# Optimization experiments

Measured on AMD Instinct MI355X. Metric: run time of the kernel, lower is better.

The kernel has to match this reference:

```python
import jax, jax.numpy as jnp
import numpy as np
from jax import lax

EMBED = 200
HID = 300
NCLASS = 2
B = 64
S = 255          # complete binary tree: 2**8 - 1 nodes
DEPTH = 8        # levels 0..7, root at node 0
VOCAB = 32000


def make_tree():
    parent = np.zeros(S, np.int32)
    parent[0] = S  # sentinel: root has no parent (dropped via dummy segment)
    for i in range(1, S):
        parent[i] = (i - 1) // 2
    depth = np.floor(np.log2(np.arange(S) + 1)).astype(np.int32)
    return jnp.asarray(parent), jnp.asarray(depth)


def setup_inputs() -> dict:
    key = jax.random.key(0)
    ks = jax.random.split(key, 8)
    parent, depth = make_tree()
    return {
        "x": jax.random.randint(ks[0], (S, B), 0, VOCAB, dtype=jnp.int32),
        "parent": parent,
        "depth": depth,
        "embed": jax.random.normal(ks[1], (VOCAB, EMBED), jnp.float32) * 0.1,
        "W_iou": jax.random.normal(ks[2], (EMBED, 3 * HID), jnp.float32) * 0.05,
        "U_iou": jax.random.normal(ks[3], (HID, 3 * HID), jnp.float32) * 0.05,
        "b_iou": jnp.zeros((3 * HID,), jnp.float32),
        "W_f": jax.random.normal(ks[4], (EMBED, HID), jnp.float32) * 0.05,
        "U_f": jax.random.normal(ks[5], (HID, HID), jnp.float32) * 0.05,
        "b_f": jnp.zeros((HID,), jnp.float32),
        "W_out": jax.random.normal(ks[6], (HID, NCLASS), jnp.float32) * 0.05,
        "b_out": jnp.zeros((NCLASS,), jnp.float32),
    }


def reference(x, parent, depth, embed, W_iou, U_iou, b_iou, W_f, U_f, b_f, W_out, b_out):
    # x: [S, B] token ids (seq-major, as in the torch model)
    emb = embed[x]                              # [S, B, E]
    wx_iou = emb @ W_iou + b_iou                # [S, B, 3H] input contributions
    wx_f = emb @ W_f + b_f                      # [S, B, H]
    seg = jnp.minimum(parent, S)                # root -> dummy segment S
    pidx = jnp.clip(parent, 0, S - 1)           # safe gather index for parent's x-part

    H0 = jnp.zeros((S, B, HID), emb.dtype)
    C0 = jnp.zeros((S, B, HID), emb.dtype)

    def level_step(carry, d):
        H, C = carry
        child = (depth == d + 1)[:, None, None].astype(H.dtype)   # nodes feeding level d
        # child-sum of hidden states into parents
        h_sum = jax.ops.segment_sum(H * child, seg, num_segments=S + 1)[:S]  # [S,B,H]
        # per-child forget gate: sigma(W_f x_parent + U_f h_child + b_f)
        f = jax.nn.sigmoid(wx_f[pidx] + H @ U_f)                  # [S,B,H]
        fc = jax.ops.segment_sum(f * C * child, seg, num_segments=S + 1)[:S]
        iou = wx_iou + h_sum @ U_iou                              # [S,B,3H]
        i_g, o_g, u_g = jnp.split(iou, 3, axis=-1)
        i_g = jax.nn.sigmoid(i_g)
        o_g = jax.nn.sigmoid(o_g)
        u_g = jnp.tanh(u_g)
        c_new = i_g * u_g + fc
        h_new = o_g * jnp.tanh(c_new)
        node = (depth == d)[:, None, None]
        H = jnp.where(node, h_new, H)
        C = jnp.where(node, c_new, C)
        return (H, C), None

    levels = jnp.arange(DEPTH - 1, -1, -1)      # process deepest level first
    (H, C), _ = lax.scan(level_step, (H0, C0), levels)

    tree_hidden = H[0]                          # [B, H] root hidden state
    logits = tree_hidden @ W_out + b_out        # Linear(hidden_dim, n_class)
    return jax.nn.log_softmax(logits, axis=-1)  # [B, 2]
```

## Files before the change

### kernel.cpp

```cpp
#include <hip/hip_runtime.h>
#include <hip/hip_bf16.h>
#include <math.h>

#define NS 255
#define NB 64
#define NE 200
#define NH 300
#define TS 2048
#define HTS 1024


typedef __attribute__((ext_vector_type(8))) short short8;
typedef __attribute__((ext_vector_type(4))) float f32x4;

__device__ __forceinline__ float sigmoidf_(float x) { return 1.0f / (1.0f + __expf(-x)); }
__device__ __forceinline__ unsigned short f2bf(float v) {
    union { __hip_bfloat16 b; unsigned short u; } cv; cv.b = __float2bfloat16(v); return cv.u;
}
__device__ __forceinline__ float bf2f(unsigned short u) {
    union { unsigned short u; __hip_bfloat16 b; } cv; cv.u = u; return __bfloat162float(cv.b);
}
__device__ __forceinline__ unsigned short f2h(float v) {
    union { _Float16 h; unsigned short u; } cv; cv.h = (_Float16)v; return cv.u;
}
__device__ __forceinline__ float h2f(unsigned short u) {
    union { unsigned short u; _Float16 h; } cv; cv.u = u; return (float)cv.h;
}
__device__ __forceinline__ int swz(int row, int kk) {
    int g = (kk >> 3) ^ ((row >> 1) & 3);
    return ((row << 2) + g) * 8 + (kk & 7);
}

__global__ __launch_bounds__(256) void prep_kernel(
    const float* __restrict__ U_iou, const float* __restrict__ U_f,
    const float* __restrict__ W_iou, const float* __restrict__ W_f,
    const float* __restrict__ embed, const int* __restrict__ x,
    unsigned short* __restrict__ BW, unsigned short* __restrict__ AembT)
{
    const int gBW = 4 * 5 * 17 * 256;
    const int gAe = NS * 7 * 256;
    int total = gBW + gAe;
    int stride = gridDim.x * blockDim.x;
    for (int gi = blockIdx.x * blockDim.x + threadIdx.x; gi < total; gi += stride) {
        unsigned short st[8];
        if (gi < gBW) {
            int gg = gi & 255, tile = gi >> 8;
            int row = gg >> 2, pos = gg & 3;
            int kk0 = (pos ^ ((row >> 1) & 3)) << 3;
            int c = tile % 17, t2 = tile / 17;
            int s = t2 % 5, g4 = t2 / 5;
            int j = s * 64 + row;
#pragma unroll
            for (int u = 0; u < 8; ++u) {
                int kk = kk0 + u; float v = 0.f;
                if (c < 7) {
                    int k = c * 32 + kk;
                    if (j < NH && k < NE)
                        v = (g4 < 3) ? W_iou[k * 900 + g4 * NH + j] : W_f[k * NH + j];
                } else {
                    int k = (c - 7) * 32 + kk;
                    if (j < NH && k < NH)
                        v = (g4 < 3) ? U_iou[k * 900 + g4 * NH + j] : U_f[k * NH + j];
                }
                st[u] = f2bf(v);
            }
            *(short8*)(BW + (size_t)tile * TS + (row * 4 + pos) * 8) = *(short8*)st;
        } else {
            int gi2 = gi - gBW;
            int gg = gi2 & 255, tile = gi2 >> 8;
            int row = gg >> 2, pos = gg & 3;
            int kk0 = (pos ^ ((row >> 1) & 3)) << 3;
            int c = tile % 7, node = tile / 7;
            int k0 = c * 32 + kk0;
            const float* er = embed + (size_t)x[node * NB + row] * NE;
#pragma unroll
            for (int u = 0; u < 8; ++u)
                st[u] = (k0 + u < NE) ? f2bf(er[k0 + u]) : (unsigned short)0;
            *(short8*)(AembT + (size_t)tile * TS + (row * 4 + pos) * 8) = *(short8*)st;
        }
    }
}

template<int NCH, int SA>
__device__ __forceinline__ void gemm2(f32x4 acc[4][2],
    const unsigned short* __restrict__ A, const unsigned short* __restrict__ B)
{
#pragma unroll
    for (int c = 0; c < NCH; ++c) {
        const unsigned short* At = A + c * SA;
        const unsigned short* Bt = B + c * TS;
        short8 a0 = *(const short8*)(At);
        short8 a1 = *(const short8*)(At + 512);
#pragma unroll
        for (int t = 0; t < 4; ++t) {
            short8 b = *(const short8*)(Bt + t * 512);
            acc[t][0] = __builtin_amdgcn_mfma_f32_16x16x32_bf16(a0, b, acc[t][0], 0, 0, 0);
            acc[t][1] = __builtin_amdgcn_mfma_f32_16x16x32_bf16(a1, b, acc[t][1], 0, 0, 0);
        }
    }
}
template<int NCH>
__device__ __forceinline__ void gemm_f(f32x4 acc[4][4],
    const unsigned short* __restrict__ A, const unsigned short* __restrict__ B)
{
#pragma unroll
    for (int c = 0; c < NCH; ++c) {
        const unsigned short* At = A + c * TS;
        const unsigned short* Bt = B + c * TS;
        short8 a0 = *(const short8*)(At);
        short8 a1 = *(const short8*)(At + 512);
        short8 a2 = *(const short8*)(At + 1024);
        short8 a3 = *(const short8*)(At + 1536);
#pragma unroll
        for (int t = 0; t < 4; ++t) {
            short8 b = *(const short8*)(Bt + t * 512);
            acc[t][0] = __builtin_amdgcn_mfma_f32_16x16x32_bf16(a0, b, acc[t][0], 0, 0, 0);
            acc[t][1] = __builtin_amdgcn_mfma_f32_16x16x32_bf16(a1, b, acc[t][1], 0, 0, 0);
            acc[t][2] = __builtin_amdgcn_mfma_f32_16x16x32_bf16(a2, b, acc[t][2], 0, 0, 0);
            acc[t][3] = __builtin_amdgcn_mfma_f32_16x16x32_bf16(a3, b, acc[t][3], 0, 0, 0);
        }
    }
}

__global__ __launch_bounds__(320) void level_kernel(
    const unsigned short* __restrict__ AembT, const unsigned short* __restrict__ BW,
    const float* __restrict__ b_iou, const float* __restrict__ b_f,
    unsigned short* __restrict__ HbfT, unsigned short* __restrict__ Cg,
    int base, int m, int sh)
{
    __shared__ unsigned short sm[24 * HTS];
    int bid = blockIdx.x;
    int p, s, half;
    if (m > 0) {
        int xcd = bid & 7, idx = bid >> 3;
        int o = idx % m, rest = idx / m;
        p = base + xcd * m + o;
        s = rest % 5; half = rest / 5;
    } else {
        int xcd = bid & 7;
        if (xcd & ((1 << sh) - 1)) return;
        p = base + (xcd >> sh);
        int idx = bid >> 3;
        s = idx % 5; half = idx / 5;
    }
    int tid = threadIdx.x;
    int w = tid >> 6, lane = tid & 63, ln = lane & 15, quad = lane >> 4;
    int l = 2 * p + 1, r = 2 * p + 2;
    int bsel = (w < 4) ? w : 3;
    int gq = (quad ^ ((ln >> 1) & 3)) * 8;
    int offA = (half * 32 + ln) * 32 + gq;
    int offL = ln * 32 + gq;
    int offB = ln * 32 + gq;

    for (int idx = w; idx < 24; idx += 5) {
        const unsigned short* gsrc;
        if (idx < 20) {
            int node = (idx < 10) ? l : r;
            int tt = (idx < 10) ? idx : idx - 10;
            gsrc = HbfT + ((size_t)node * 10 + tt) * TS + half * HTS;
        } else {
            int ii = idx - 20;
            int node = (ii < 2) ? l : r;
            gsrc = Cg + ((size_t)node * 10 + 2 * s + (ii & 1)) * TS + half * HTS;
        }
        unsigned short* ldst = sm + idx * HTS;
#pragma unroll
        for (int u = 0; u < 2; ++u)
            __builtin_amdgcn_global_load_lds(
                (const __attribute__((address_space(1))) unsigned short*)(gsrc + u * 512 + lane * 8),
                (__attribute__((address_space(3))) unsigned short*)(ldst + u * 512 + lane * 8),
                16, 0, 0);
    }

    f32x4 acc[4][2];
#pragma unroll
    for (int t = 0; t < 4; ++t)
#pragma unroll
        for (int q = 0; q < 2; ++q) acc[t][q] = (f32x4){0.f, 0.f, 0.f, 0.f};

    const unsigned short* Bsrc = BW + (size_t)(bsel * 5 + s) * 17 * TS;
    const unsigned short* Ae = AembT + (size_t)p * 7 * TS;
    gemm2<7, TS>(acc, Ae + offA, Bsrc + offB);

    __syncthreads();

    const unsigned short* BH = Bsrc + 7 * TS + offB;
    if (w < 3) {
        gemm2<10, HTS>(acc, sm + offL, BH);
        gemm2<10, HTS>(acc, sm + 10 * HTS + offL, BH);
    } else if (w == 3) {
        gemm2<10, HTS>(acc, sm + offL, BH);
    } else {
        gemm2<10, HTS>(acc, sm + 10 * HTS + offL, BH);
    }

    float* smf = (float*)sm;
    for (int t = 0; t < 4; ++t) {
        __syncthreads();
#pragma unroll
        for (int ms = 0; ms < 2; ++ms)
#pragma unroll
            for (int rr = 0; rr < 4; ++rr)
                smf[w * 544 + (ms * 16 + quad * 4 + rr) * 17 + ln] = acc[t][ms][rr];
        __syncthreads();
        for (int idx2 = tid; idx2 < 512; idx2 += 320) {
            int mm = idx2 >> 4, n = idx2 & 15;
            int gm = half * 32 + mm;
            int jj = s * 64 + t * 16 + n;
            bool ok = jj < NH;
            float pi = smf[0 * 544 + mm * 17 + n] + (ok ? b_iou[jj] : 0.f);
            float po = smf[1 * 544 + mm * 17 + n] + (ok ? b_iou[NH + jj] : 0.f);
            float pu = smf[2 * 544 + mm * 17 + n] + (ok ? b_iou[2 * NH + jj] : 0.f);
            float bj = ok ? b_f[jj] : 0.f;
            float fl = sigmoidf_(smf[3 * 544 + mm * 17 + n] + bj);
            float fr = sigmoidf_(smf[4 * 544 + mm * 17 + n] + bj);
            int xr = (mm >> 1) & 3;
            int cel = (mm * 4 + ((((t & 1) * 2) + (n >> 3)) ^ xr)) * 8 + (n & 7);
            int ts2 = t >> 1;
            float cl = h2f(sm[(20 + ts2) * HTS + cel]);
            float cr = h2f(sm[(22 + ts2) * HTS + cel]);
            float cc = sigmoidf_(pi) * tanhf(pu) + fl * cl + fr * cr;
            float hh = sigmoidf_(po) * tanhf(cc);
            size_t tbase = ((size_t)p * 10 + (jj >> 5)) * TS + swz(gm, jj & 31);
            if (ok) Cg[tbase] = f2h(cc);
            HbfT[tbase] = ok ? f2bf(hh) : (unsigned short)0;
        }
    }
}

__global__ __launch_bounds__(192) void leaf_kernel(
    const unsigned short* __restrict__ AembT, const unsigned short* __restrict__ BW,
    const float* __restrict__ b_iou,
    unsigned short* __restrict__ HbfT, unsigned short* __restrict__ Cg, int m)
{
    int bid = blockIdx.x;
    int xcd = bid & 7, idx = bid >> 3;
    int o = idx % m, rest = idx / m;
    int p = 127 + xcd * m + o;
    int s = rest % 5;
    int tid = threadIdx.x;
    int w = tid >> 6, lane = tid & 63, ln = lane & 15, quad = lane >> 4;
    int off = ln * 32 + (quad ^ ((ln >> 1) & 3)) * 8;

    const unsigned short* Bsrc = BW + (size_t)(w * 5 + s) * 17 * TS;
    const unsigned short* Ae = AembT + (size_t)p * 7 * TS;

    f32x4 acc[4][4];
#pragma unroll
    for (int t = 0; t < 4; ++t)
#pragma unroll
        for (int q = 0; q < 4; ++q) acc[t][q] = (f32x4){0.f, 0.f, 0.f, 0.f};

    gemm_f<7>(acc, Ae + off, Bsrc + off);

    __shared__ float tile[3][64][16];
    for (int t = 0; t < 4; ++t) {
        __syncthreads();
#pragma unroll
        for (int ms = 0; ms < 4; ++ms)
#pragma unroll
            for (int rr = 0; rr < 4; ++rr)
                tile[w][ms * 16 + quad * 4 + rr][ln] = acc[t][ms][rr];
        __syncthreads();
        for (int idx2 = tid; idx2 < 1024; idx2 += 192) {
            int mm = idx2 >> 4, n = idx2 & 15;
            int jj = s * 64 + t * 16 + n;
            bool ok = jj < NH;
            float pi = tile[0][mm][n] + (ok ? b_iou[jj] : 0.f);
            float po = tile[1][mm][n] + (ok ? b_iou[NH + jj] : 0.f);
            float pu = tile[2][mm][n] + (ok ? b_iou[2 * NH + jj] : 0.f);
            float cc = sigmoidf_(pi) * tanhf(pu);
            float hh = sigmoidf_(po) * tanhf(cc);
            size_t tbase = ((size_t)p * 10 + (jj >> 5)) * TS + swz(mm, jj & 31);
            if (ok) Cg[tbase] = f2h(cc);
            HbfT[tbase] = ok ? f2bf(hh) : (unsigned short)0;
        }
    }
}

__global__ __launch_bounds__(64) void out_kernel(
    const unsigned short* __restrict__ HbfT,
    const float* __restrict__ W_out, const float* __restrict__ b_out,
    float* __restrict__ out)
{
    int b = threadIdx.x;
    float l0 = 0.f, l1 = 0.f;
#pragma unroll 4
    for (int k = 0; k < NH; ++k) {
        float hk = bf2f(HbfT[(size_t)(k >> 5) * TS + swz(b, k & 31)]);
        l0 += hk * W_out[k * 2];
        l1 += hk * W_out[k * 2 + 1];
    }
    l0 += b_out[0];
    l1 += b_out[1];
    float m = fmaxf(l0, l1);
    float lse = m + logf(__expf(l0 - m) + __expf(l1 - m));
    out[b * 2 + 0] = l0 - lse;
    out[b * 2 + 1] = l1 - lse;
}

extern "C" void kernel_launch(void* const* d_in, const int* in_sizes, int n_in,
                              void* d_out, int out_size, void* d_ws, size_t ws_size,
                              hipStream_t stream)
{
    const int*   x     = (const int*)d_in[0];
    const float* embed = (const float*)d_in[3];
    const float* W_iou = (const float*)d_in[4];
    const float* U_iou = (const float*)d_in[5];
    const float* b_iou = (const float*)d_in[6];
    const float* W_f   = (const float*)d_in[7];
    const float* U_f   = (const float*)d_in[8];
    const float* b_f   = (const float*)d_in[9];
    const float* W_out = (const float*)d_in[10];
    const float* b_out = (const float*)d_in[11];

    char* ws = (char*)d_ws;
    unsigned short* HbfT  = (unsigned short*)(ws + 0);
    unsigned short* Cg    = (unsigned short*)(ws + 10444800);
    unsigned short* AembT = (unsigned short*)(ws + 20889600);
    unsigned short* BW    = (unsigned short*)(ws + 28200960);

    prep_kernel<<<4096, 256, 0, stream>>>(U_iou, U_f, W_iou, W_f, embed, x, BW, AembT);

    leaf_kernel<<<640, 192, 0, stream>>>(AembT, BW, b_iou, HbfT, Cg, 16);
    for (int d = 6; d >= 3; --d) {
        int base = (1 << d) - 1;
        int m = 1 << (d - 3);
        level_kernel<<<80 * m, 320, 0, stream>>>(AembT, BW, b_iou, b_f, HbfT, Cg,
                                                 base, m, 0);
    }
    for (int d = 2; d >= 0; --d) {
        level_kernel<<<80, 320, 0, stream>>>(AembT, BW, b_iou, b_f, HbfT, Cg,
                                             (1 << d) - 1, 0, 3 - d);
    }
    out_kernel<<<1, 64, 0, stream>>>(HbfT, W_out, b_out, (float*)d_out);
}
```

Before: 271.0 us.

## Fuse leaf, level and output kernels into one persistent kernel with grid barriers

Replaces the separate leaf, per-level and output launches with a single persistent kernel of 256 blocks. Levels are separated by an atomic-counter grid barrier, and results are written with agent-scope relaxed atomic stores so other blocks can see them. The goal is to remove the launch gaps and tail idle time of roughly nine small dependent launches. In exchange it relies on every block being resident at once and on a spin barrier with a timeout. The leaf stage also now runs in 320-thread blocks in which two warps sit idle during the GEMM.

```diff
diff --git a/kernel.cpp b/kernel.cpp
--- a/kernel.cpp
+++ b/kernel.cpp
@@ -8,6 +8,7 @@
 #define NH 300
 #define TS 2048
 #define HTS 1024
+#define GRID 256
 
 
 typedef __attribute__((ext_vector_type(8))) short short8;
@@ -29,14 +30,19 @@
 __device__ __forceinline__ int swz(int row, int kk) {
     int g = (kk >> 3) ^ ((row >> 1) & 3);
     return ((row << 2) + g) * 8 + (kk & 7);
+}
+__device__ __forceinline__ void st_agent(unsigned short* p, unsigned short v) {
+    __hip_atomic_store(p, v, __ATOMIC_RELAXED, __HIP_MEMORY_SCOPE_AGENT);
 }
 
 __global__ __launch_bounds__(256) void prep_kernel(
     const float* __restrict__ U_iou, const float* __restrict__ U_f,
     const float* __restrict__ W_iou, const float* __restrict__ W_f,
     const float* __restrict__ embed, const int* __restrict__ x,
-    unsigned short* __restrict__ BW, unsigned short* __restrict__ AembT)
-{
+    unsigned short* __restrict__ BW, unsigned short* __restrict__ AembT,
+    unsigned int* __restrict__ ctr)
+{
+    if (blockIdx.x == 0 && threadIdx.x == 0) *ctr = 0;
     const int gBW = 4 * 5 * 17 * 256;
     const int gAe = NS * 7 * 256;
     int total = gBW + gAe;
@@ -122,27 +128,30 @@
     }
 }
 
-__global__ __launch_bounds__(320) void level_kernel(
+__device__ __forceinline__ void gsync(unsigned int* ctr, unsigned int target)
+{
+    __syncthreads();
+    if (threadIdx.x == 0) {
+        __threadfence();
+        atomicAdd(ctr, 1u);
+        int it = 0;
+        while (atomicCAS(ctr, 0xFFFFFFFFu, 0xFFFFFFFFu) < target) {
+            __builtin_amdgcn_s_sleep(8);
+            if (++it > (1 << 17)) break;
+        }
+        __threadfence();
+    }
+    __syncthreads();
+}
+
+__device__ __forceinline__ void level_body(int p, int s, int half,
     const unsigned short* __restrict__ AembT, const unsigned short* __restrict__ BW,
     const float* __restrict__ b_iou, const float* __restrict__ b_f,
     unsigned short* __restrict__ HbfT, unsigned short* __restrict__ Cg,
-    int base, int m, int sh)
-{
-    __shared__ unsigned short sm[24 * HTS];
-    int bid = blockIdx.x;
-    int p, s, half;
-    if (m > 0) {
-        int xcd = bid & 7, idx = bid >> 3;
-        int o = idx % m, rest = idx / m;
-        p = base + xcd * m + o;
-        s = rest % 5; half = rest / 5;
-    } else {
-        int xcd = bid & 7;
-        if (xcd & ((1 << sh) - 1)) return;
-        p = base + (xcd >> sh);
-        int idx = bid >> 3;
-        s = idx % 5; half = idx / 5;
-    }
+    unsigned short* sm)
+{
+    __syncthreads();
+
     int tid = threadIdx.x;
     int w = tid >> 6, lane = tid & 63, ln = lane & 15, quad = lane >> 4;
     int l = 2 * p + 1, r = 2 * p + 2;
@@ -152,18 +161,18 @@
     int offL = ln * 32 + gq;
     int offB = ln * 32 + gq;
 
-    for (int idx = w; idx < 24; idx += 5) {
+    for (int sidx = w; sidx < 24; sidx += 5) {
         const unsigned short* gsrc;
-        if (idx < 20) {
-            int node = (idx < 10) ? l : r;
-            int tt = (idx < 10) ? idx : idx - 10;
+        if (sidx < 20) {
+            int node = (sidx < 10) ? l : r;
+            int tt = (sidx < 10) ? sidx : sidx - 10;
             gsrc = HbfT + ((size_t)node * 10 + tt) * TS + half * HTS;
         } else {
-            int ii = idx - 20;
+            int ii = sidx - 20;
             int node = (ii < 2) ? l : r;
             gsrc = Cg + ((size_t)node * 10 + 2 * s + (ii & 1)) * TS + half * HTS;
         }
-        unsigned short* ldst = sm + idx * HTS;
+        unsigned short* ldst = sm + sidx * HTS;
 #pragma unroll
         for (int u = 0; u < 2; ++u)
             __builtin_amdgcn_global_load_lds(
@@ -222,81 +231,129 @@
             float cc = sigmoidf_(pi) * tanhf(pu) + fl * cl + fr * cr;
             float hh = sigmoidf_(po) * tanhf(cc);
             size_t tbase = ((size_t)p * 10 + (jj >> 5)) * TS + swz(gm, jj & 31);
-            if (ok) Cg[tbase] = f2h(cc);
-            HbfT[tbase] = ok ? f2bf(hh) : (unsigned short)0;
-        }
-    }
-}
-
-__global__ __launch_bounds__(192) void leaf_kernel(
+            if (ok) st_agent(Cg + tbase, f2h(cc));
+            st_agent(HbfT + tbase, ok ? f2bf(hh) : (unsigned short)0);
+        }
+    }
+}
+
+__device__ __forceinline__ void leaf_body(int p, int s,
     const unsigned short* __restrict__ AembT, const unsigned short* __restrict__ BW,
     const float* __restrict__ b_iou,
-    unsigned short* __restrict__ HbfT, unsigned short* __restrict__ Cg, int m)
-{
-    int bid = blockIdx.x;
-    int xcd = bid & 7, idx = bid >> 3;
-    int o = idx % m, rest = idx / m;
-    int p = 127 + xcd * m + o;
-    int s = rest % 5;
+    unsigned short* __restrict__ HbfT, unsigned short* __restrict__ Cg,
+    unsigned short* sm)
+{
     int tid = threadIdx.x;
     int w = tid >> 6, lane = tid & 63, ln = lane & 15, quad = lane >> 4;
     int off = ln * 32 + (quad ^ ((ln >> 1) & 3)) * 8;
-
-    const unsigned short* Bsrc = BW + (size_t)(w * 5 + s) * 17 * TS;
+    int wb = (w < 3) ? w : 0;
+    const unsigned short* Bsrc = BW + (size_t)(wb * 5 + s) * 17 * TS;
     const unsigned short* Ae = AembT + (size_t)p * 7 * TS;
 
     f32x4 acc[4][4];
-#pragma unroll
-    for (int t = 0; t < 4; ++t)
-#pragma unroll
-        for (int q = 0; q < 4; ++q) acc[t][q] = (f32x4){0.f, 0.f, 0.f, 0.f};
-
-    gemm_f<7>(acc, Ae + off, Bsrc + off);
-
-    __shared__ float tile[3][64][16];
+    if (w < 3) {
+#pragma unroll
+        for (int t = 0; t < 4; ++t)
+#pragma unroll
+            for (int q = 0; q < 4; ++q) acc[t][q] = (f32x4){0.f, 0.f, 0.f, 0.f};
+        gemm_f<7>(acc, Ae + off, Bsrc + off);
+    }
+
+    float* tf = (float*)sm;
     for (int t = 0; t < 4; ++t) {
         __syncthreads();
-#pragma unroll
-        for (int ms = 0; ms < 4; ++ms)
-#pragma unroll
-            for (int rr = 0; rr < 4; ++rr)
-                tile[w][ms * 16 + quad * 4 + rr][ln] = acc[t][ms][rr];
-        __syncthreads();
-        for (int idx2 = tid; idx2 < 1024; idx2 += 192) {
+        if (w < 3)
+#pragma unroll
+            for (int ms = 0; ms < 4; ++ms)
+#pragma unroll
+                for (int rr = 0; rr < 4; ++rr)
+                    tf[(w * 64 + ms * 16 + quad * 4 + rr) * 16 + ln] = acc[t][ms][rr];
+        __syncthreads();
+        for (int idx2 = tid; idx2 < 1024; idx2 += 320) {
             int mm = idx2 >> 4, n = idx2 & 15;
             int jj = s * 64 + t * 16 + n;
             bool ok = jj < NH;
-            float pi = tile[0][mm][n] + (ok ? b_iou[jj] : 0.f);
-            float po = tile[1][mm][n] + (ok ? b_iou[NH + jj] : 0.f);
-            float pu = tile[2][mm][n] + (ok ? b_iou[2 * NH + jj] : 0.f);
+            float pi = tf[(0 * 64 + mm) * 16 + n] + (ok ? b_iou[jj] : 0.f);
+            float po = tf[(1 * 64 + mm) * 16 + n] + (ok ? b_iou[NH + jj] : 0.f);
+            float pu = tf[(2 * 64 + mm) * 16 + n] + (ok ? b_iou[2 * NH + jj] : 0.f);
             float cc = sigmoidf_(pi) * tanhf(pu);
             float hh = sigmoidf_(po) * tanhf(cc);
             size_t tbase = ((size_t)p * 10 + (jj >> 5)) * TS + swz(mm, jj & 31);
-            if (ok) Cg[tbase] = f2h(cc);
-            HbfT[tbase] = ok ? f2bf(hh) : (unsigned short)0;
-        }
-    }
-}
-
-__global__ __launch_bounds__(64) void out_kernel(
-    const unsigned short* __restrict__ HbfT,
+            if (ok) st_agent(Cg + tbase, f2h(cc));
+            st_agent(HbfT + tbase, ok ? f2bf(hh) : (unsigned short)0);
+        }
+    }
+}
+
+__global__ __launch_bounds__(320, 2) void tree_kernel(
+    const unsigned short* __restrict__ AembT, const unsigned short* __restrict__ BW,
+    const float* __restrict__ b_iou, const float* __restrict__ b_f,
+    unsigned short* __restrict__ HbfT, unsigned short* __restrict__ Cg,
     const float* __restrict__ W_out, const float* __restrict__ b_out,
-    float* __restrict__ out)
-{
-    int b = threadIdx.x;
-    float l0 = 0.f, l1 = 0.f;
+    float* __restrict__ outp, unsigned int* __restrict__ ctr)
+{
+    __shared__ unsigned short sm[24 * HTS];
+    int bid = blockIdx.x;
+    int tid = threadIdx.x;
+    unsigned int tgt = GRID;
+
+    for (int T = bid; T < 640; T += GRID) {
+        int xcd = T & 7, idx = T >> 3;
+        leaf_body(127 + xcd * 16 + (idx & 15), idx >> 4,
+                  AembT, BW, b_iou, HbfT, Cg, sm);
+    }
+    gsync(ctr, tgt); tgt += GRID;
+
+#pragma unroll 1
+    for (int d = 6; d >= 3; --d) {
+        int sh2 = d - 3;
+        int ntask = 80 << sh2;
+        for (int T = bid; T < ntask; T += GRID) {
+            int xcd = T & 7, idx = T >> 3;
+            int o = idx & ((1 << sh2) - 1);
+            int rest = idx >> sh2;
+            level_body((1 << d) - 1 + (xcd << sh2) + o, rest % 5, rest / 5,
+                       AembT, BW, b_iou, b_f, HbfT, Cg, sm);
+        }
+        gsync(ctr, tgt); tgt += GRID;
+    }
+
+#pragma unroll 1
+    for (int d = 2; d >= 0; --d) {
+        int ntask = 10 << d;
+        if (bid < ntask) {
+            int rest = bid % 10;
+            level_body((1 << d) - 1 + bid / 10, rest % 5, rest / 5,
+                       AembT, BW, b_iou, b_f, HbfT, Cg, sm);
+        }
+        gsync(ctr, tgt); tgt += GRID;
+    }
+
+    if (bid != 0) return;
+    {
+        float* wsm = (float*)(sm + 20 * HTS);
+        for (int i = tid; i < 2560; i += 320)
+            *(short8*)(sm + i * 8) = *(const short8*)(HbfT + i * 8);
+        for (int i = tid; i < 2 * NH; i += 320)
+            wsm[i] = W_out[i];
+        __syncthreads();
+        if (tid < 64) {
+            int b = tid;
+            float l0 = 0.f, l1 = 0.f;
 #pragma unroll 4
-    for (int k = 0; k < NH; ++k) {
-        float hk = bf2f(HbfT[(size_t)(k >> 5) * TS + swz(b, k & 31)]);
-        l0 += hk * W_out[k * 2];
-        l1 += hk * W_out[k * 2 + 1];
-    }
-    l0 += b_out[0];
-    l1 += b_out[1];
-    float m = fmaxf(l0, l1);
-    float lse = m + logf(__expf(l0 - m) + __expf(l1 - m));
-    out[b * 2 + 0] = l0 - lse;
-    out[b * 2 + 1] = l1 - lse;
+            for (int k = 0; k < NH; ++k) {
+                float hk = bf2f(sm[(k >> 5) * TS + swz(b, k & 31)]);
+                l0 += hk * wsm[2 * k];
+                l1 += hk * wsm[2 * k + 1];
+            }
+            l0 += b_out[0];
+            l1 += b_out[1];
+            float mx = fmaxf(l0, l1);
+            float lse = mx + logf(__expf(l0 - mx) + __expf(l1 - mx));
+            outp[b * 2 + 0] = l0 - lse;
+            outp[b * 2 + 1] = l1 - lse;
+        }
+    }
 }
 
 extern "C" void kernel_launch(void* const* d_in, const int* in_sizes, int n_in,
@@ -319,19 +376,10 @@
     unsigned short* Cg    = (unsigned short*)(ws + 10444800);
     unsigned short* AembT = (unsigned short*)(ws + 20889600);
     unsigned short* BW    = (unsigned short*)(ws + 28200960);
-
-    prep_kernel<<<4096, 256, 0, stream>>>(U_iou, U_f, W_iou, W_f, embed, x, BW, AembT);
-
-    leaf_kernel<<<640, 192, 0, stream>>>(AembT, BW, b_iou, HbfT, Cg, 16);
-    for (int d = 6; d >= 3; --d) {
-        int base = (1 << d) - 1;
-        int m = 1 << (d - 3);
-        level_kernel<<<80 * m, 320, 0, stream>>>(AembT, BW, b_iou, b_f, HbfT, Cg,
-                                                 base, m, 0);
-    }
-    for (int d = 2; d >= 0; --d) {
-        level_kernel<<<80, 320, 0, stream>>>(AembT, BW, b_iou, b_f, HbfT, Cg,
-                                             (1 << d) - 1, 0, 3 - d);
-    }
-    out_kernel<<<1, 64, 0, stream>>>(HbfT, W_out, b_out, (float*)d_out);
-}
+    unsigned int*   ctr   = (unsigned int*)(ws + 29593600);
+
+    prep_kernel<<<4096, 256, 0, stream>>>(U_iou, U_f, W_iou, W_f, embed, x,
+                                          BW, AembT, ctr);
+    tree_kernel<<<GRID, 320, 0, stream>>>(AembT, BW, b_iou, b_f, HbfT, Cg,
+                                          W_out, b_out, (float*)d_out, ctr);
+}
```

Result: slower. 505.0 us (+86.4%).
